# Kernel tuning notes

Hardware: AMD Instinct MI355X
Metric: run time of the kernel (lower is better)

The kernel has to match this reference:

```python
import jax, jax.numpy as jnp
import numpy as np

N, E = 40000, 640000
EMB, HID, H, TXT = 128, 128, 4, 384
C = HID // H  # per-head channels = 32


def _prelu(x, a):
    return jnp.where(x >= 0, x, a * x)


def _layernorm(x, g, b, eps=1e-5):
    m = jnp.mean(x, axis=-1, keepdims=True)
    v = jnp.mean((x - m) ** 2, axis=-1, keepdims=True)
    return (x - m) / jnp.sqrt(v + eps) * g + b


def _gat_conv(h, src, dst, W, att_src, att_dst, bias):
    # PyG GATConv (concat=True, eval mode): lin has no bias, self-loops already in src/dst.
    xh = (h @ W.T).reshape(N, H, C)                      # [N,H,C]
    a_src = jnp.sum(xh * att_src, axis=-1)               # [N,H]
    a_dst = jnp.sum(xh * att_dst, axis=-1)               # [N,H]
    alpha = jax.nn.leaky_relu(a_src[src] + a_dst[dst], negative_slope=0.2)  # [Et,H]
    amax = jax.ops.segment_max(alpha, dst, num_segments=N)
    ex = jnp.exp(alpha - amax[dst])
    denom = jax.ops.segment_sum(ex, dst, num_segments=N)
    coef = ex / denom[dst]                               # scatter-softmax over dst
    out = jax.ops.segment_sum(xh[src] * coef[:, :, None], dst, num_segments=N)
    return out.reshape(N, H * C) + bias


def setup_inputs() -> dict:
    key = jax.random.key(0)
    ks = jax.random.split(key, 20)
    nrm = lambda k, s, sc=0.05: jax.random.normal(k, s, jnp.float32) * sc
    inp = {
        "x": nrm(ks[0], (N, EMB), 1.0),
        "num_x": nrm(ks[1], (N, 1), 1.0),
        "num_mask": jnp.ones((N,), jnp.float32),
        "txt_x": nrm(ks[2], (N, TXT), 1.0),
        "txt_mask": jnp.ones((N,), jnp.float32),
        "edge_index": jax.random.randint(ks[3], (2, E), 0, N, jnp.int32),
        "num_proj_w": nrm(ks[4], (EMB, 1)), "num_proj_b": jnp.zeros((EMB,), jnp.float32),
        "txt_proj_w": nrm(ks[5], (EMB, TXT)), "txt_proj_b": jnp.zeros((EMB,), jnp.float32),
        "node_proj_w": nrm(ks[6], (HID, EMB)), "node_proj_b": jnp.zeros((HID,), jnp.float32),
        "prelu0_a": jnp.full((HID,), 0.25, jnp.float32),
        "conv1_w": nrm(ks[7], (HID, HID)), "att_src1": nrm(ks[8], (H, C)), "att_dst1": nrm(ks[9], (H, C)), "bias1": jnp.zeros((HID,), jnp.float32),
        "norm1_g": jnp.ones((HID,), jnp.float32), "norm1_b": jnp.zeros((HID,), jnp.float32),
        "prelu1_a": jnp.full((HID,), 0.25, jnp.float32),
        "conv2_w": nrm(ks[10], (HID, HID)), "att_src2": nrm(ks[11], (H, C)), "att_dst2": nrm(ks[12], (H, C)), "bias2": jnp.zeros((HID,), jnp.float32),
        "norm2_g": jnp.ones((HID,), jnp.float32), "norm2_b": jnp.zeros((HID,), jnp.float32),
        "prelu2_a": jnp.full((HID,), 0.25, jnp.float32),
        "out_w": nrm(ks[13], (1, HID)), "out_b": jnp.zeros((1,), jnp.float32),
    }
    return inp


def reference(x, num_x, num_mask, txt_x, txt_mask, edge_index,
              num_proj_w, num_proj_b, txt_proj_w, txt_proj_b,
              node_proj_w, node_proj_b, prelu0_a,
              conv1_w, att_src1, att_dst1, bias1, norm1_g, norm1_b, prelu1_a,
              conv2_w, att_src2, att_dst2, bias2, norm2_g, norm2_b, prelu2_a,
              out_w, out_b):
    # add self loops (PyG GATConv default)
    loop = jnp.arange(N, dtype=edge_index.dtype)
    src = jnp.concatenate([edge_index[0], loop])
    dst = jnp.concatenate([edge_index[1], loop])

    h = (num_x * num_mask[:, None]) @ num_proj_w.T + num_proj_b
    h = h + (txt_x * txt_mask[:, None]) @ txt_proj_w.T + txt_proj_b
    h = h + x @ node_proj_w.T + node_proj_b
    h = _prelu(h, prelu0_a)

    h = _gat_conv(h, src, dst, conv1_w, att_src1, att_dst1, bias1)
    h = _prelu(_layernorm(h, norm1_g, norm1_b), prelu1_a)  # dropout: eval mode -> identity

    h = _gat_conv(h, src, dst, conv2_w, att_src2, att_dst2, bias2)
    h = _prelu(_layernorm(h, norm2_g, norm2_b), prelu2_a)

    return (h @ out_w.T + out_b).squeeze(-1)  # [N]
```

## Files before the change

kernel.cpp:

```cpp
#include <hip/hip_runtime.h>
#include <stdint.h>

typedef unsigned short u16;
typedef unsigned int u32;
typedef __attribute__((ext_vector_type(8))) short bf16x8;
typedef __attribute__((ext_vector_type(4))) float f32x4;

__device__ __forceinline__ float bf2f(u32 u) {
    union { u32 i; float f; } v; v.i = u << 16; return v.f;
}
__device__ __forceinline__ u16 f2bf(float f) {
    u32 x = __float_as_uint(f);
    return (u16)((x + 0x7fffu + ((x >> 16) & 1u)) >> 16);
}
__device__ __forceinline__ float wred_sum(float v) {
#pragma unroll
    for (int o = 32; o > 0; o >>= 1) v += __shfl_xor(v, o, 64);
    return v;
}
__device__ __forceinline__ bf16x8 cvt8(float4 a, float4 b) {
    union { uint4 u; bf16x8 v; } t;
    t.u.x = (u32)f2bf(a.x) | ((u32)f2bf(a.y) << 16);
    t.u.y = (u32)f2bf(a.z) | ((u32)f2bf(a.w) << 16);
    t.u.z = (u32)f2bf(b.x) | ((u32)f2bf(b.y) << 16);
    t.u.w = (u32)f2bf(b.z) | ((u32)f2bf(b.w) << 16);
    return t.v;
}
__device__ __forceinline__ bf16x8 ld16B(const u16* p, size_t off) {
    union { uint4 u; bf16x8 b; } t; t.u = *(const uint4*)(p + off); return t.b;
}
__device__ __forceinline__ void glds16(const void* g, void* l) {
    __builtin_amdgcn_global_load_lds(
        (const __attribute__((address_space(1))) void*)g,
        (__attribute__((address_space(3))) void*)l, 16, 0, 0);
}
__device__ __forceinline__ void stageW_glds(const u16* __restrict__ W, int ldk, int koff,
                                            u16* swl, int tid) {
    int w64 = tid >> 6;
#pragma unroll
    for (int it = 0; it < 8; ++it) {
        int row = it * 16 + (tid >> 4);
        int sphys = tid & 15;
        int ssrc = sphys ^ (row & 7);
        const u16* g = W + (size_t)row * ldk + koff + ssrc * 8;
        u16* dst = swl + (size_t)(it * 256 + w64 * 64) * 8;
        glds16(g, dst);
    }
}
__device__ __forceinline__ bf16x8 ldBx(const u16* swl, int ct, int ks, int l16, int quad) {
    int row = ct * 16 + l16;
    int slot = (ks * 4 + quad) ^ (row & 7);
    union { uint4 u; bf16x8 b; } t;
    t.u = *(const uint4*)&swl[row * 128 + slot * 8];
    return t.b;
}
__device__ __forceinline__ void stageA_glds(const float* __restrict__ Ab, int ldk, int koff,
                                            float* sAw, int lane) {
#pragma unroll
    for (int it = 0; it < 8; ++it) {
        int rl = it * 2 + (lane >> 5);
        int sl = (lane & 31) ^ (rl & 7);
        const float* g = Ab + (size_t)rl * ldk + koff + sl * 4;
        glds16(g, sAw + it * 256);
    }
}

__global__ void k_cvtw(const float* __restrict__ s0, const float* __restrict__ s1,
                       const float* __restrict__ s2, const float* __restrict__ s3,
                       u16* __restrict__ d, int n0, int n1, int n2, int n3) {
    int i = (blockIdx.x * 256 + threadIdx.x) * 8;
    int t = i;
    const float* s;
    if (t < n0) s = s0 + t;
    else if ((t -= n0) < n1) s = s1 + t;
    else if ((t -= n1) < n2) s = s2 + t;
    else if ((t -= n2) < n3) s = s3 + t;
    else return;
    float4 a = *(const float4*)s, b = *(const float4*)(s + 4);
    uint4 v;
    v.x = (u32)f2bf(a.x) | ((u32)f2bf(a.y) << 16);
    v.y = (u32)f2bf(a.z) | ((u32)f2bf(a.w) << 16);
    v.z = (u32)f2bf(b.x) | ((u32)f2bf(b.y) << 16);
    v.w = (u32)f2bf(b.z) | ((u32)f2bf(b.w) << 16);
    *(uint4*)(d + i) = v;
}

__global__ void k_zero(int* __restrict__ p, int n) {
    int i = blockIdx.x * 256 + threadIdx.x;
    if (i < n) p[i] = 0;
}
__global__ void k_hist(const int* __restrict__ dst, int E, int* __restrict__ deg) {
    int e = blockIdx.x * 256 + threadIdx.x;
    if (e < E) atomicAdd(&deg[dst[e]], 1);
}
__global__ __launch_bounds__(1024) void k_scanA(const int* __restrict__ deg, int n,
                                                int* __restrict__ out, int* __restrict__ bsum) {
    __shared__ int wsum[16];
    int t = threadIdx.x, w = t >> 6, lane = t & 63;
    int i0 = blockIdx.x * 4096 + t * 4;
    int4 v = make_int4(0, 0, 0, 0);
    if (i0 + 3 < n) v = *(const int4*)&deg[i0];
    else {
        if (i0 < n)     v.x = deg[i0];
        if (i0 + 1 < n) v.y = deg[i0 + 1];
        if (i0 + 2 < n) v.z = deg[i0 + 2];
    }
    int tsum = v.x + v.y + v.z + v.w;
    int s = tsum;
#pragma unroll
    for (int o = 1; o < 64; o <<= 1) { int u = __shfl_up(s, o, 64); if (lane >= o) s += u; }
    if (lane == 63) wsum[w] = s;
    __syncthreads();
    if (w == 0 && lane < 16) {
        int ws = wsum[lane];
#pragma unroll
        for (int o = 1; o < 16; o <<= 1) { int u = __shfl_up(ws, o, 64); if (lane >= o) ws += u; }
        wsum[lane] = ws;
    }
    __syncthreads();
    int woff = (w == 0) ? 0 : wsum[w - 1];
    int p = woff + s - tsum;
    if (i0 + 3 < n) {
        int4 o4; o4.x = p; o4.y = p + v.x; o4.z = p + v.x + v.y; o4.w = p + v.x + v.y + v.z;
        *(int4*)&out[i0] = o4;
    } else {
        int pp = p;
        if (i0 < n)     { out[i0] = pp;     pp += v.x; }
        if (i0 + 1 < n) { out[i0 + 1] = pp; pp += v.y; }
        if (i0 + 2 < n) { out[i0 + 2] = pp; }
    }
    if (t == 0) bsum[blockIdx.x] = wsum[15];
}
__global__ void k_scanB(int* __restrict__ bsum, int nb, int* __restrict__ total) {
    int lane = threadIdx.x;
    int v = (lane < nb) ? bsum[lane] : 0;
    int s = v;
#pragma unroll
    for (int o = 1; o < 64; o <<= 1) { int u = __shfl_up(s, o, 64); if (lane >= o) s += u; }
    if (lane < nb) bsum[lane] = s - v;
    if (lane == 63) total[0] = s;
}
__global__ void k_scanC(int* __restrict__ rowptr, int* __restrict__ cursor,
                        const int* __restrict__ boff, int n) {
    int i = blockIdx.x * 256 + threadIdx.x;
    if (i < n) {
        int r = rowptr[i] + boff[i >> 12];
        rowptr[i] = r; cursor[i] = r;
    }
}
__global__ void k_scatter(const int* __restrict__ srcp, const int* __restrict__ dstp, int E,
                          int* __restrict__ cursor, int* __restrict__ col) {
    int e = blockIdx.x * 256 + threadIdx.x;
    if (e < E) {
        int p = atomicAdd(&cursor[dstp[e]], 1);
        col[p] = srcp[e];
    }
}

__global__ __launch_bounds__(256) void k_fused1(
    const float* __restrict__ x, const float* __restrict__ numx, const float* __restrict__ numm,
    const float* __restrict__ txt, const float* __restrict__ txtm,
    const float* __restrict__ numw, const float* __restrict__ numb,
    const float* __restrict__ txtb, const float* __restrict__ nodeb,
    const float* __restrict__ pa,
    const u16* __restrict__ txtwb, const u16* __restrict__ nodewb, const u16* __restrict__ w1b,
    const float* __restrict__ atts, const float* __restrict__ attd,
    u16* __restrict__ xh, float* __restrict__ asrc, float* __restrict__ adst) {
    __shared__ u16 swl[128 * 128];
    __shared__ float sA[4][2048];
    int tid = threadIdx.x, w = tid >> 6, lane = tid & 63, quad = lane >> 4, l16 = lane & 15;
    int nb = blockIdx.x * 64 + w * 16;

    float* sAw = &sA[w][0];
    u16* shw = (u16*)sAw;
    const float* tBase = txt + (size_t)nb * 384;
    const float* xBase = x + (size_t)nb * 128;

    f32x4 acc[8];
#pragma unroll
    for (int ct = 0; ct < 8; ++ct) { f32x4 z = {0.f, 0.f, 0.f, 0.f}; acc[ct] = z; }

#define CHUNK(Wp, ldk, koff, Ab)                                                \
    {                                                                           \
        stageW_glds(Wp, ldk, koff, swl, tid);                                   \
        stageA_glds(Ab, ldk, koff, sAw, lane);                                  \
        __syncthreads();                              \
        _Pragma("unroll")                                                       \
        for (int ks = 0; ks < 4; ++ks) {                                        \
            int s0 = (ks * 8 + quad * 2) ^ (l16 & 7);                           \
            int s1 = (ks * 8 + quad * 2 + 1) ^ (l16 & 7);                       \
            float4 fa = *(const float4*)&sAw[l16 * 128 + s0 * 4];               \
            float4 fb = *(const float4*)&sAw[l16 * 128 + s1 * 4];               \
            bf16x8 a0 = cvt8(fa, fb);                                           \
            _Pragma("unroll")                                                   \
            for (int ct = 0; ct < 8; ++ct)                                      \
                acc[ct] = __builtin_amdgcn_mfma_f32_16x16x32_bf16(              \
                    a0, ldBx(swl, ct, ks, l16, quad), acc[ct], 0, 0, 0);        \
        }                                                                       \
        __syncthreads();                        \
    }

    CHUNK(txtwb, 384, 0,   tBase)
    CHUNK(txtwb, 384, 128, tBase)
    CHUNK(txtwb, 384, 256, tBase)
#pragma unroll
    for (int r = 0; r < 4; ++r) {
        float tm = txtm[nb + quad * 4 + r];
#pragma unroll
        for (int ct = 0; ct < 8; ++ct) acc[ct][r] *= tm;
    }
    CHUNK(nodewb, 128, 0, xBase)
#undef CHUNK

    float nm[4];
#pragma unroll
    for (int r = 0; r < 4; ++r) {
        int n = nb + quad * 4 + r;
        nm[r] = numx[n] * numm[n];
    }
#pragma unroll
    for (int ct = 0; ct < 8; ++ct) {
        int c = ct * 16 + l16;
        float cw = numw[c];
        float cb = numb[c] + txtb[c] + nodeb[c];
        float pav = pa[c];
#pragma unroll
        for (int r = 0; r < 4; ++r) {
            float v = acc[ct][r] + nm[r] * cw + cb;
            v = v >= 0.f ? v : pav * v;
            int rr = quad * 4 + r;
            int ps = (c >> 3) ^ (rr & 7);
            shw[rr * 128 + ps * 8 + (c & 7)] = f2bf(v);
        }
    }
    __syncthreads();
    stageW_glds(w1b, 128, 0, swl, tid);
    __syncthreads();
    f32x4 a2[8];
#pragma unroll
    for (int ct = 0; ct < 8; ++ct) { f32x4 z = {0.f, 0.f, 0.f, 0.f}; a2[ct] = z; }
#pragma unroll
    for (int ks = 0; ks < 4; ++ks) {
        bf16x8 a0 = ld16B(shw, l16 * 128 + (((ks * 4 + quad) ^ (l16 & 7)) << 3));
#pragma unroll
        for (int ct = 0; ct < 8; ++ct)
            a2[ct] = __builtin_amdgcn_mfma_f32_16x16x32_bf16(
                a0, ldBx(swl, ct, ks, l16, quad), a2[ct], 0, 0, 0);
    }
#pragma unroll
    for (int ct = 0; ct < 8; ++ct) {
        int c = ct * 16 + l16;
#pragma unroll
        for (int r = 0; r < 4; ++r)
            xh[(size_t)(nb + quad * 4 + r) * 128 + c] = f2bf(a2[ct][r]);
    }
    float as_[8], ad_[8];
#pragma unroll
    for (int ct = 0; ct < 8; ++ct) {
        int c = ct * 16 + l16;
        as_[ct] = atts[c];
        ad_[ct] = attd[c];
    }
#pragma unroll
    for (int hh = 0; hh < 4; ++hh) {
        float vs[4], vd[4];
#pragma unroll
        for (int r = 0; r < 4; ++r) {
            vs[r] = a2[2 * hh][r] * as_[2 * hh] + a2[2 * hh + 1][r] * as_[2 * hh + 1];
            vd[r] = a2[2 * hh][r] * ad_[2 * hh] + a2[2 * hh + 1][r] * ad_[2 * hh + 1];
        }
#pragma unroll
        for (int o = 1; o <= 8; o <<= 1) {
#pragma unroll
            for (int r = 0; r < 4; ++r) {
                vs[r] += __shfl_xor(vs[r], o, 64);
                vd[r] += __shfl_xor(vd[r], o, 64);
            }
        }
        if ((l16 >> 2) == hh) {
            int r = l16 & 3;
            float ss = (r == 0) ? vs[0] : (r == 1) ? vs[1] : (r == 2) ? vs[2] : vs[3];
            float dd = (r == 0) ? vd[0] : (r == 1) ? vd[1] : (r == 2) ? vd[2] : vd[3];
            int n = nb + quad * 4 + r;
            asrc[n * 4 + hh] = ss;
            adst[n * 4 + hh] = dd;
        }
    }
}

__global__ __launch_bounds__(256) void k_xh(
    const u16* __restrict__ h, const u16* __restrict__ Wb,
    const float* __restrict__ att_s, const float* __restrict__ att_d,
    u16* __restrict__ xh, float* __restrict__ asrc, float* __restrict__ adst) {
    __shared__ u16 swl[128 * 128];
    int tid = threadIdx.x;
    int w = tid >> 6, lane = tid & 63, quad = lane >> 4, l16 = lane & 15;
    int nb = blockIdx.x * 64 + w * 16;

    stageW_glds(Wb, 128, 0, swl, tid);
    const u16* hrow = h + (size_t)(nb + l16) * 128 + quad * 8;
    uint4 A0 = *(const uint4*)(hrow);
    uint4 A1 = *(const uint4*)(hrow + 32);
    uint4 A2 = *(const uint4*)(hrow + 64);
    uint4 A3 = *(const uint4*)(hrow + 96);
    f32x4 acc[8];
#pragma unroll
    for (int ct = 0; ct < 8; ++ct) { f32x4 z = {0.f, 0.f, 0.f, 0.f}; acc[ct] = z; }
    __syncthreads();
    union { uint4 u; bf16x8 b; } t0, t1, t2, t3;
    t0.u = A0; t1.u = A1; t2.u = A2; t3.u = A3;
#pragma unroll
    for (int ct = 0; ct < 8; ++ct)
        acc[ct] = __builtin_amdgcn_mfma_f32_16x16x32_bf16(
            t0.b, ldBx(swl, ct, 0, l16, quad), acc[ct], 0, 0, 0);
#pragma unroll
    for (int ct = 0; ct < 8; ++ct)
        acc[ct] = __builtin_amdgcn_mfma_f32_16x16x32_bf16(
            t1.b, ldBx(swl, ct, 1, l16, quad), acc[ct], 0, 0, 0);
#pragma unroll
    for (int ct = 0; ct < 8; ++ct)
        acc[ct] = __builtin_amdgcn_mfma_f32_16x16x32_bf16(
            t2.b, ldBx(swl, ct, 2, l16, quad), acc[ct], 0, 0, 0);
#pragma unroll
    for (int ct = 0; ct < 8; ++ct)
        acc[ct] = __builtin_amdgcn_mfma_f32_16x16x32_bf16(
            t3.b, ldBx(swl, ct, 3, l16, quad), acc[ct], 0, 0, 0);
#pragma unroll
    for (int ct = 0; ct < 8; ++ct) {
        int c = ct * 16 + l16;
#pragma unroll
        for (int r = 0; r < 4; ++r) {
            int n = nb + quad * 4 + r;
            xh[(size_t)n * 128 + c] = f2bf(acc[ct][r]);
        }
    }
    float as_[8], ad_[8];
#pragma unroll
    for (int ct = 0; ct < 8; ++ct) {
        int c = ct * 16 + l16;
        as_[ct] = att_s[c];
        ad_[ct] = att_d[c];
    }
#pragma unroll
    for (int hh = 0; hh < 4; ++hh) {
        float vs[4], vd[4];
#pragma unroll
        for (int r = 0; r < 4; ++r) {
            vs[r] = acc[2 * hh][r] * as_[2 * hh] + acc[2 * hh + 1][r] * as_[2 * hh + 1];
            vd[r] = acc[2 * hh][r] * ad_[2 * hh] + acc[2 * hh + 1][r] * ad_[2 * hh + 1];
        }
#pragma unroll
        for (int o = 1; o <= 8; o <<= 1) {
#pragma unroll
            for (int r = 0; r < 4; ++r) {
                vs[r] += __shfl_xor(vs[r], o, 64);
                vd[r] += __shfl_xor(vd[r], o, 64);
            }
        }
        if ((l16 >> 2) == hh) {
            int r = l16 & 3;
            float ss = (r == 0) ? vs[0] : (r == 1) ? vs[1] : (r == 2) ? vs[2] : vs[3];
            float dd = (r == 0) ? vd[0] : (r == 1) ? vd[1] : (r == 2) ? vd[2] : vd[3];
            int n = nb + quad * 4 + r;
            asrc[n * 4 + hh] = ss;
            adst[n * 4 + hh] = dd;
        }
    }
}

__global__ __launch_bounds__(64) void k_agg(
    const u16* __restrict__ xh, const float* __restrict__ asrc, const float* __restrict__ adst,
    const int* __restrict__ rowptr, const int* __restrict__ col,
    const float* __restrict__ bias, const float* __restrict__ g, const float* __restrict__ b,
    const float* __restrict__ pa, u16* __restrict__ hnext,
    const float* __restrict__ outw, const float* __restrict__ outb, float* __restrict__ outy,
    int is_final) {
    __shared__ int   scol[64];
    __shared__ float scoef[64][4];
    int n = blockIdx.x, lane = threadIdx.x;
    int beg = rowptr[n], end = rowptr[n + 1];
    const float4* asrc4 = (const float4*)asrc;

    float4 adv = ((const float4*)adst)[n];
    float ad[4] = { adv.x, adv.y, adv.z, adv.w };
    float4 asv = asrc4[n];
    float els[4];
#pragma unroll
    for (int h = 0; h < 4; h++) {
        float a = ((const float*)&asv)[h] + ad[h];
        a = a >= 0.f ? a : 0.2f * a;
        els[h] = __expf(a);
    }
    int hh = lane >> 4;
    u32 vself = ((const u32*)(xh + (size_t)n * 128))[lane];
    float ac0[8], ac1[8];
#pragma unroll
    for (int q = 0; q < 8; ++q) { ac0[q] = 0.f; ac1[q] = 0.f; }
    ac0[0] = els[hh] * bf2f(vself & 0xffffu);
    ac1[0] = els[hh] * bf2f(vself >> 16);
    float l[4] = { 0.f, 0.f, 0.f, 0.f };

    for (int base = beg; base < end; base += 64) {
        int e = base + lane;
        int cnt = min(64, end - base);
        if (e < end) {
            int s = col[e];
            float4 av = asrc4[s];
            scol[lane] = s;
            float cf[4];
#pragma unroll
            for (int h = 0; h < 4; h++) {
                float a = ((const float*)&av)[h] + ad[h];
                a = a >= 0.f ? a : 0.2f * a;
                cf[h] = __expf(a);
                l[h] += cf[h];
            }
            *(float4*)scoef[lane] = make_float4(cf[0], cf[1], cf[2], cf[3]);
        }
        __syncthreads();
        int j = 0;
        for (; j + 7 < cnt; j += 8) {
            int ss[8]; float cc[8]; u32 vv[8];
#pragma unroll
            for (int q = 0; q < 8; ++q) { ss[q] = scol[j + q]; cc[q] = scoef[j + q][hh]; }
#pragma unroll
            for (int q = 0; q < 8; ++q) vv[q] = ((const u32*)(xh + (size_t)ss[q] * 128))[lane];
#pragma unroll
            for (int q = 0; q < 8; ++q) {
                ac0[q] += cc[q] * bf2f(vv[q] & 0xffffu);
                ac1[q] += cc[q] * bf2f(vv[q] >> 16);
            }
        }
        for (; j + 3 < cnt; j += 4) {
            int ss[4]; float cc[4]; u32 vv[4];
#pragma unroll
            for (int q = 0; q < 4; ++q) { ss[q] = scol[j + q]; cc[q] = scoef[j + q][hh]; }
#pragma unroll
            for (int q = 0; q < 4; ++q) vv[q] = ((const u32*)(xh + (size_t)ss[q] * 128))[lane];
#pragma unroll
            for (int q = 0; q < 4; ++q) {
                ac0[q] += cc[q] * bf2f(vv[q] & 0xffffu);
                ac1[q] += cc[q] * bf2f(vv[q] >> 16);
            }
        }
        for (; j < cnt; ++j) {
            int s0 = scol[j];
            float c0 = scoef[j][hh];
            u32 v0 = ((const u32*)(xh + (size_t)s0 * 128))[lane];
            ac0[0] += c0 * bf2f(v0 & 0xffffu);
            ac1[0] += c0 * bf2f(v0 >> 16);
        }
        __syncthreads();
    }
    float acc0 = 0.f, acc1 = 0.f;
#pragma unroll
    for (int q = 0; q < 8; ++q) { acc0 += ac0[q]; acc1 += ac1[q]; }

    float L[4];
#pragma unroll
    for (int h = 0; h < 4; h++) L[h] = wred_sum(l[h]) + els[h];
    float inv = 1.f / L[hh];
    acc0 *= inv;
    acc1 *= inv;

    int c0i = 2 * lane;
    float2 bi = *(const float2*)(bias + c0i);
    acc0 += bi.x; acc1 += bi.y;

    float mean = wred_sum(acc0 + acc1) * (1.f / 128.f);
    float d0 = acc0 - mean, d1 = acc1 - mean;
    float var = wred_sum(d0 * d0 + d1 * d1) * (1.f / 128.f);
    float rstd = rsqrtf(var + 1e-5f);
    float2 gg = *(const float2*)(g + c0i);
    float2 bb = *(const float2*)(b + c0i);
    float2 pp = *(const float2*)(pa + c0i);
    float y0 = d0 * rstd * gg.x + bb.x;
    float y1 = d1 * rstd * gg.y + bb.y;
    y0 = y0 >= 0.f ? y0 : pp.x * y0;
    y1 = y1 >= 0.f ? y1 : pp.y * y1;

    if (is_final) {
        float2 ow = *(const float2*)(outw + c0i);
        float dot = wred_sum(y0 * ow.x + y1 * ow.y);
        if (lane == 0) outy[n] = dot + outb[0];
    } else {
        ((u32*)(hnext + (size_t)n * 128))[lane] = (u32)f2bf(y0) | ((u32)f2bf(y1) << 16);
    }
}

extern "C" void kernel_launch(void* const* d_in, const int* in_sizes, int n_in,
                              void* d_out, int out_size, void* d_ws, size_t ws_size,
                              hipStream_t stream) {
    const int N = in_sizes[2];
    const int E = in_sizes[5] / 2;

    const float* x      = (const float*)d_in[0];
    const float* numx   = (const float*)d_in[1];
    const float* numm   = (const float*)d_in[2];
    const float* txt    = (const float*)d_in[3];
    const float* txtm   = (const float*)d_in[4];
    const int*   ei     = (const int*)d_in[5];
    const float* numw   = (const float*)d_in[6];
    const float* numb   = (const float*)d_in[7];
    const float* txtw   = (const float*)d_in[8];
    const float* txtb   = (const float*)d_in[9];
    const float* nodew  = (const float*)d_in[10];
    const float* nodeb  = (const float*)d_in[11];
    const float* pa0    = (const float*)d_in[12];
    const float* conv1w = (const float*)d_in[13];
    const float* atts1  = (const float*)d_in[14];
    const float* attd1  = (const float*)d_in[15];
    const float* bias1  = (const float*)d_in[16];
    const float* g1     = (const float*)d_in[17];
    const float* b1     = (const float*)d_in[18];
    const float* pa1    = (const float*)d_in[19];
    const float* conv2w = (const float*)d_in[20];
    const float* atts2  = (const float*)d_in[21];
    const float* attd2  = (const float*)d_in[22];
    const float* bias2  = (const float*)d_in[23];
    const float* g2     = (const float*)d_in[24];
    const float* b2     = (const float*)d_in[25];
    const float* pa2    = (const float*)d_in[26];
    const float* outw   = (const float*)d_in[27];
    const float* outb   = (const float*)d_in[28];

    const int* srcp = ei;
    const int* dstp = ei + E;

    const int szTxtw = in_sizes[8];
    const int szNode = in_sizes[10];
    const int szW1   = in_sizes[13];
    const int szW2   = in_sizes[20];
    const int szWAll = szTxtw + szNode + szW1 + szW2;

    char* p = (char*)d_ws;
    auto alloc = [&](size_t bytes) -> void* {
        void* q = (void*)p;
        p += (bytes + 255) & ~(size_t)255;
        return q;
    };
    u16*   hA     = (u16*)alloc((size_t)N * 128 * 2);
    u16*   hB     = (u16*)alloc((size_t)N * 128 * 2);
    float* asrc   = (float*)alloc((size_t)N * 4 * 4);
    float* adst   = (float*)alloc((size_t)N * 4 * 4);
    int*   deg    = (int*)alloc((size_t)N * 4);
    int*   rowptr = (int*)alloc((size_t)(N + 1) * 4);
    int*   cursor = (int*)alloc((size_t)N * 4);
    int*   col    = (int*)alloc((size_t)E * 4);
    int*   bsum   = (int*)alloc(64 * 4);
    u16*   wbf    = (u16*)alloc((size_t)szWAll * 2);

    u16* txtwb  = wbf;
    u16* nodewb = wbf + szTxtw;
    u16* w1b    = nodewb + szNode;
    u16* w2b    = w1b + szW1;

    k_cvtw<<<(szWAll / 8 + 255) / 256, 256, 0, stream>>>(
        txtw, nodew, conv1w, conv2w, wbf, szTxtw, szNode, szW1, szW2);

    const int nbScan = (N + 4095) / 4096;
    k_zero<<<(N + 255) / 256, 256, 0, stream>>>(deg, N);
    k_hist<<<(E + 255) / 256, 256, 0, stream>>>(dstp, E, deg);
    k_scanA<<<nbScan, 1024, 0, stream>>>(deg, N, rowptr, bsum);
    k_scanB<<<1, 64, 0, stream>>>(bsum, nbScan, rowptr + N);
    k_scanC<<<(N + 255) / 256, 256, 0, stream>>>(rowptr, cursor, bsum, N);
    k_scatter<<<(E + 255) / 256, 256, 0, stream>>>(srcp, dstp, E, cursor, col);

    const int gProj = N / 64;

    k_fused1<<<gProj, 256, 0, stream>>>(x, numx, numm, txt, txtm, numw, numb,
                                        txtb, nodeb, pa0,
                                        txtwb, nodewb, w1b, atts1, attd1, hB, asrc, adst);
    k_agg<<<N, 64, 0, stream>>>(hB, asrc, adst, rowptr, col, bias1, g1, b1, pa1,
                                hA, nullptr, nullptr, nullptr, 0);

    k_xh<<<gProj, 256, 0, stream>>>(hA, w2b, atts2, attd2, hB, asrc, adst);
    k_agg<<<N, 64, 0, stream>>>(hB, asrc, adst, rowptr, col, bias2, g2, b2, pa2,
                                nullptr, outw, outb, (float*)d_out, 1);
}
```

Before: 318.9 us.

## Double-buffer weight tiles and load activations directly to registers in fused projection

The fused input-projection kernel now double-buffers the weight tile in LDS, so the next chunk's weights stream in while MFMAs run on the current chunk. Activation rows are read straight from global memory into registers instead of being staged through LDS, and the intermediate bf16 tile uses a padded stride of 136 instead of an XOR swizzle. This removes a barrier per chunk and overlaps loads with compute. In exchange it raises register pressure from the prefetched float4 sets and keeps LDS use the same at 64KB.

New measurement: 324.0 us. Within noise of the previous version (+1.6%).

```diff
diff --git a/kernel.cpp b/kernel.cpp
--- a/kernel.cpp
+++ b/kernel.cpp
@@ -53,16 +53,6 @@
     union { uint4 u; bf16x8 b; } t;
     t.u = *(const uint4*)&swl[row * 128 + slot * 8];
     return t.b;
-}
-__device__ __forceinline__ void stageA_glds(const float* __restrict__ Ab, int ldk, int koff,
-                                            float* sAw, int lane) {
-#pragma unroll
-    for (int it = 0; it < 8; ++it) {
-        int rl = it * 2 + (lane >> 5);
-        int sl = (lane & 31) ^ (rl & 7);
-        const float* g = Ab + (size_t)rl * ldk + koff + sl * 4;
-        glds16(g, sAw + it * 256);
-    }
 }
 
 __global__ void k_cvtw(const float* __restrict__ s0, const float* __restrict__ s1,
@@ -166,87 +156,116 @@
     const u16* __restrict__ txtwb, const u16* __restrict__ nodewb, const u16* __restrict__ w1b,
     const float* __restrict__ atts, const float* __restrict__ attd,
     u16* __restrict__ xh, float* __restrict__ asrc, float* __restrict__ adst) {
-    __shared__ u16 swl[128 * 128];
-    __shared__ float sA[4][2048];
+    __shared__ u16 swl[2][128 * 128];
     int tid = threadIdx.x, w = tid >> 6, lane = tid & 63, quad = lane >> 4, l16 = lane & 15;
     int nb = blockIdx.x * 64 + w * 16;
 
-    float* sAw = &sA[w][0];
-    u16* shw = (u16*)sAw;
-    const float* tBase = txt + (size_t)nb * 384;
-    const float* xBase = x + (size_t)nb * 128;
+    const float* trow = txt + (size_t)(nb + l16) * 384 + quad * 8;
+    const float* xrow = x + (size_t)(nb + l16) * 128 + quad * 8;
 
     f32x4 acc[8];
 #pragma unroll
     for (int ct = 0; ct < 8; ++ct) { f32x4 z = {0.f, 0.f, 0.f, 0.f}; acc[ct] = z; }
 
-#define CHUNK(Wp, ldk, koff, Ab)                                                \
+#define LDA(P, base)                                                            \
+    float4 P##0 = *(const float4*)((base) + 0),  P##1 = *(const float4*)((base) + 4);   \
+    float4 P##2 = *(const float4*)((base) + 32), P##3 = *(const float4*)((base) + 36);  \
+    float4 P##4 = *(const float4*)((base) + 64), P##5 = *(const float4*)((base) + 68);  \
+    float4 P##6 = *(const float4*)((base) + 96), P##7 = *(const float4*)((base) + 100);
+
+#define COMPUTE(buf, P)                                                         \
     {                                                                           \
-        stageW_glds(Wp, ldk, koff, swl, tid);                                   \
-        stageA_glds(Ab, ldk, koff, sAw, lane);                                  \
-        __syncthreads();                              \
+        bf16x8 f0_ = cvt8(P##0, P##1), f1_ = cvt8(P##2, P##3);                  \
+        bf16x8 f2_ = cvt8(P##4, P##5), f3_ = cvt8(P##6, P##7);                  \
         _Pragma("unroll")                                                       \
-        for (int ks = 0; ks < 4; ++ks) {                                        \
-            int s0 = (ks * 8 + quad * 2) ^ (l16 & 7);                           \
-            int s1 = (ks * 8 + quad * 2 + 1) ^ (l16 & 7);                       \
-            float4 fa = *(const float4*)&sAw[l16 * 128 + s0 * 4];               \
-            float4 fb = *(const float4*)&sAw[l16 * 128 + s1 * 4];               \
-            bf16x8 a0 = cvt8(fa, fb);                                           \
-            _Pragma("unroll")                                                   \
-            for (int ct = 0; ct < 8; ++ct)                                      \
-                acc[ct] = __builtin_amdgcn_mfma_f32_16x16x32_bf16(              \
-                    a0, ldBx(swl, ct, ks, l16, quad), acc[ct], 0, 0, 0);        \
-        }                                                                       \
-        __syncthreads();                        \
-    }
-
-    CHUNK(txtwb, 384, 0,   tBase)
-    CHUNK(txtwb, 384, 128, tBase)
-    CHUNK(txtwb, 384, 256, tBase)
+        for (int ct = 0; ct < 8; ++ct)                                          \
+            acc[ct] = __builtin_amdgcn_mfma_f32_16x16x32_bf16(                  \
+                f0_, ldBx(buf, ct, 0, l16, quad), acc[ct], 0, 0, 0);            \
+        _Pragma("unroll")                                                       \
+        for (int ct = 0; ct < 8; ++ct)                                          \
+            acc[ct] = __builtin_amdgcn_mfma_f32_16x16x32_bf16(                  \
+                f1_, ldBx(buf, ct, 1, l16, quad), acc[ct], 0, 0, 0);            \
+        _Pragma("unroll")                                                       \
+        for (int ct = 0; ct < 8; ++ct)                                          \
+            acc[ct] = __builtin_amdgcn_mfma_f32_16x16x32_bf16(                  \
+                f2_, ldBx(buf, ct, 2, l16, quad), acc[ct], 0, 0, 0);            \
+        _Pragma("unroll")                                                       \
+        for (int ct = 0; ct < 8; ++ct)                                          \
+            acc[ct] = __builtin_amdgcn_mfma_f32_16x16x32_bf16(                  \
+                f3_, ldBx(buf, ct, 3, l16, quad), acc[ct], 0, 0, 0);            \
+    }
+
+    stageW_glds(txtwb, 384, 0, swl[0], tid);
+    LDA(Aa, trow)
+    __syncthreads();
+
+    stageW_glds(txtwb, 384, 128, swl[1], tid);
+    LDA(Ab, trow + 128)
+    COMPUTE(swl[0], Aa)
+    __syncthreads();
+
+    stageW_glds(txtwb, 384, 256, swl[0], tid);
+    LDA(Ac, trow + 256)
+    COMPUTE(swl[1], Ab)
+    __syncthreads();
+
+    stageW_glds(nodewb, 128, 0, swl[1], tid);
+    LDA(Ad, xrow)
+    COMPUTE(swl[0], Ac)
 #pragma unroll
     for (int r = 0; r < 4; ++r) {
         float tm = txtm[nb + quad * 4 + r];
 #pragma unroll
         for (int ct = 0; ct < 8; ++ct) acc[ct][r] *= tm;
     }
-    CHUNK(nodewb, 128, 0, xBase)
-#undef CHUNK
-
-    float nm[4];
-#pragma unroll
-    for (int r = 0; r < 4; ++r) {
-        int n = nb + quad * 4 + r;
-        nm[r] = numx[n] * numm[n];
-    }
+    __syncthreads();
+
+    stageW_glds(w1b, 128, 0, swl[0], tid);
+    COMPUTE(swl[1], Ad)
+    {
+        float nm[4];
+#pragma unroll
+        for (int r = 0; r < 4; ++r) {
+            int n = nb + quad * 4 + r;
+            nm[r] = numx[n] * numm[n];
+        }
+#pragma unroll
+        for (int ct = 0; ct < 8; ++ct) {
+            int c = ct * 16 + l16;
+            float cw = numw[c];
+            float cb = numb[c] + txtb[c] + nodeb[c];
+            float pav = pa[c];
+#pragma unroll
+            for (int r = 0; r < 4; ++r) {
+                float v = acc[ct][r] + nm[r] * cw + cb;
+                acc[ct][r] = v >= 0.f ? v : pav * v;
+            }
+        }
+    }
+    __syncthreads();
+
+    u16* shw = ((u16*)swl[1]) + w * 16 * 136;
 #pragma unroll
     for (int ct = 0; ct < 8; ++ct) {
         int c = ct * 16 + l16;
-        float cw = numw[c];
-        float cb = numb[c] + txtb[c] + nodeb[c];
-        float pav = pa[c];
-#pragma unroll
-        for (int r = 0; r < 4; ++r) {
-            float v = acc[ct][r] + nm[r] * cw + cb;
-            v = v >= 0.f ? v : pav * v;
-            int rr = quad * 4 + r;
-            int ps = (c >> 3) ^ (rr & 7);
-            shw[rr * 128 + ps * 8 + (c & 7)] = f2bf(v);
-        }
-    }
-    __syncthreads();
-    stageW_glds(w1b, 128, 0, swl, tid);
-    __syncthreads();
+#pragma unroll
+        for (int r = 0; r < 4; ++r)
+            shw[(quad * 4 + r) * 136 + c] = f2bf(acc[ct][r]);
+    }
     f32x4 a2[8];
 #pragma unroll
     for (int ct = 0; ct < 8; ++ct) { f32x4 z = {0.f, 0.f, 0.f, 0.f}; a2[ct] = z; }
 #pragma unroll
     for (int ks = 0; ks < 4; ++ks) {
-        bf16x8 a0 = ld16B(shw, l16 * 128 + (((ks * 4 + quad) ^ (l16 & 7)) << 3));
+        bf16x8 a0 = ld16B(shw, l16 * 136 + ks * 32 + quad * 8);
 #pragma unroll
         for (int ct = 0; ct < 8; ++ct)
             a2[ct] = __builtin_amdgcn_mfma_f32_16x16x32_bf16(
-                a0, ldBx(swl, ct, ks, l16, quad), a2[ct], 0, 0, 0);
-    }
+                a0, ldBx(swl[0], ct, ks, l16, quad), a2[ct], 0, 0, 0);
+    }
+#undef LDA
+#undef COMPUTE
+
 #pragma unroll
     for (int ct = 0; ct < 8; ++ct) {
         int c = ct * 16 + l16;
```
